# Kernel tuning notes

Hardware: AMD Instinct MI355X
Metric: run time of the kernel (lower is better)

The kernel has to match this reference:

```python
import jax, jax.numpy as jnp
import numpy as np

N_NODES = 100000


def gcn_conv(x, edge_index, W, b):
    # PyG GCNConv: add self-loops, symmetric normalization, then scatter-add.
    n = x.shape[0]
    loops = jnp.arange(n, dtype=edge_index.dtype)
    src = jnp.concatenate([edge_index[0], loops])
    dst = jnp.concatenate([edge_index[1], loops])
    h = x @ W  # [N, F_out] -- transform before propagate (small GEMM)
    ones = jnp.ones(src.shape[0], dtype=x.dtype)
    deg = jax.ops.segment_sum(ones, dst, num_segments=n)  # in-degree incl. self-loop
    dinv = jnp.where(deg > 0, jax.lax.rsqrt(deg), 0.0)
    norm = dinv[src] * dinv[dst]  # [E+N]
    msg = h[src] * norm[:, None]  # gather + scale, [E+N, F_out]
    out = jax.ops.segment_sum(msg, dst, num_segments=n)  # scatter-add
    return out + b


def setup_inputs() -> dict:
    key = jax.random.key(0)
    k1, k2, k3, k4 = jax.random.split(key, 4)
    d = 128
    x = jax.random.normal(k1, (N_NODES, d), dtype=jnp.float32)
    edge_index = jax.random.randint(k2, (2, 1600000), 0, N_NODES, dtype=jnp.int64)
    scale = 1.0 / np.sqrt(d)
    W1 = jax.random.normal(k3, (d, d), dtype=jnp.float32) * scale
    b1 = jnp.zeros((d,), dtype=jnp.float32)
    W2 = jax.random.normal(k4, (d, d), dtype=jnp.float32) * scale
    b2 = jnp.zeros((d,), dtype=jnp.float32)
    return {"x": x, "edge_index": edge_index, "W1": W1, "b1": b1, "W2": W2, "b2": b2}


def reference(x, edge_index, W1, b1, W2, b2):
    # Layer 1: GCNConv -> relu -> dropout(eval: identity)
    h = jax.nn.relu(gcn_conv(x, edge_index, W1, b1))
    # Layer 2
    h = jax.nn.relu(gcn_conv(h, edge_index, W2, b2))
    return h
```

## Files before the change

### kernel.cpp

```cpp
#include <hip/hip_runtime.h>


#define NFEAT 128
#define BSH 7
#define MAXNB 1024
#define BCAP 4096
#define HP 72

typedef __attribute__((ext_vector_type(8))) short s8v;
typedef __attribute__((ext_vector_type(4))) float f4v;
typedef __attribute__((ext_vector_type(2))) float f2v;
typedef __attribute__((ext_vector_type(4))) uint u4v;

__device__ inline ushort f2bf(float f) {
    union { float f; uint u; } x; x.f = f;
    uint u = x.u;
    return (ushort)((u + 0x7fffu + ((u >> 16) & 1u)) >> 16);
}
__device__ inline f2v unpk(uint u) {
    union { uint u; float f; } lo, hi;
    lo.u = u << 16;
    hi.u = u & 0xffff0000u;
    return (f2v){lo.f, hi.f};
}
__device__ inline void upfma2(uint4 v, float g, f2v* a) {
    a[0] += g * unpk(v.x);
    a[1] += g * unpk(v.y);
    a[2] += g * unpk(v.z);
    a[3] += g * unpk(v.w);
}

template <bool ABF16>
__device__ inline void gemm_body(ushort* Bs, int bid, const void* __restrict__ Ap,
                                 const float* __restrict__ W,
                                 ushort* __restrict__ hs, int M) {
    int t = threadIdx.x;
    int w = t >> 6, l = t & 63;
    int q = l >> 4, ln = l & 15;
    int row0 = (bid * 4 + w) * 16;

    int arow = row0 + ln;
    if (arow >= M) arow = M - 1;
    s8v afr[4];
    if (ABF16) {
        const ushort* A = (const ushort*)Ap + (size_t)arow * NFEAT + q * 8;
#pragma unroll
        for (int g = 0; g < 4; g++) afr[g] = *(const s8v*)(A + g * 32);
    } else {
        const float* A = (const float*)Ap + (size_t)arow * NFEAT + q * 8;
#pragma unroll
        for (int g = 0; g < 4; g++) {
            float4 f0 = *(const float4*)(A + g * 32);
            float4 f1 = *(const float4*)(A + g * 32 + 4);
            ushort o[8] = {f2bf(f0.x), f2bf(f0.y), f2bf(f0.z), f2bf(f0.w),
                           f2bf(f1.x), f2bf(f1.y), f2bf(f1.z), f2bf(f1.w)};
            __builtin_memcpy(&afr[g], o, 16);
        }
    }

    f4v acc[8];
#pragma unroll
    for (int nt = 0; nt < 8; nt++) acc[nt] = (f4v){0.f, 0.f, 0.f, 0.f};

#pragma unroll
    for (int h = 0; h < 2; h++) {
        if (h) __syncthreads();
#pragma unroll
        for (int i = 0; i < 8; i++) {
            int idx = t + i * 256;
            int k4 = idx >> 7;
            int n = idx & 127;
            ushort o[4];
#pragma unroll
            for (int j = 0; j < 4; j++) o[j] = f2bf(W[(h * 64 + k4 * 4 + j) * NFEAT + n]);
            uint2 pk;
            __builtin_memcpy(&pk, o, 8);
            *(uint2*)&Bs[n * HP + k4 * 4] = pk;
        }
        __syncthreads();
#pragma unroll
        for (int nt = 0; nt < 8; nt++) {
            const ushort* Bp = Bs + (nt * 16 + ln) * HP + q * 8;
#pragma unroll
            for (int ks = 0; ks < 2; ks++) {
                s8v bfr = *(const s8v*)(Bp + ks * 32);
                acc[nt] = __builtin_amdgcn_mfma_f32_16x16x32_bf16(afr[h * 2 + ks], bfr, acc[nt], 0, 0, 0);
            }
        }
    }

#pragma unroll
    for (int r = 0; r < 4; r++) {
        int row = row0 + q * 4 + r;
        if (row < M) {
            ushort* hp = hs + (size_t)row * NFEAT + ln;
#pragma unroll
            for (int nt = 0; nt < 8; nt++) hp[nt * 16] = f2bf(acc[nt][r]);
        }
    }
}

__global__ __launch_bounds__(256) void k_fused1(const int* __restrict__ src,
                                                const int* __restrict__ dst,
                                                int* __restrict__ gcnt,
                                                uint* __restrict__ ebuf,
                                                int E, int NB, int CH, int chBlk,
                                                const float* __restrict__ x,
                                                const float* __restrict__ W1,
                                                ushort* __restrict__ hs, int M) {
    __shared__ __align__(16) ushort smem[128 * HP];
    int bid = blockIdx.x;
    int sid = bid / 3, r = bid % 3;
    if (r == 0 && sid < chBlk) {
        int* h = (int*)smem;
        int t = threadIdx.x;
        for (int i = t; i < NB; i += 256) h[i] = 0;
        __syncthreads();
        int e0 = sid * CH;
        int e1 = min(e0 + CH, E);
        for (int e = e0 + t; e < e1; e += 256) atomicAdd(&h[dst[e] >> BSH], 1);
        __syncthreads();
        for (int i = t; i < NB; i += 256) {
            int c = h[i];
            h[i] = c ? (i * BCAP + atomicAdd(&gcnt[i], c)) : 0;
        }
        __syncthreads();
        for (int e = e0 + t; e < e1; e += 256) {
            int d = dst[e];
            int b = d >> BSH;
            int p = atomicAdd(&h[b], 1);
            if (p < (b + 1) * BCAP)
                ebuf[p] = ((uint)src[e] << BSH) | (uint)(d & ((1 << BSH) - 1));
        }
    } else {
        int scats_before = min(sid + (r ? 1 : 0), chBlk);
        gemm_body<false>(smem, bid - scats_before, x, W1, hs, M);
    }
}

template <bool ABF16>
__global__ __launch_bounds__(256) void k_gemm3(const void* __restrict__ Ap,
                                               const float* __restrict__ W,
                                               ushort* __restrict__ hs, int M) {
    __shared__ __align__(16) ushort Bs[128 * HP];
    gemm_body<ABF16>(Bs, blockIdx.x, Ap, W, hs, M);
}

__global__ __launch_bounds__(256) void k_fill2(const uint* __restrict__ ebuf,
                                               const int* __restrict__ gcnt,
                                               int* __restrict__ row_ptr,
                                               float* __restrict__ dinv,
                                               int* __restrict__ col,
                                               int N, int E, int NB) {
    __shared__ int cnt[128];
    __shared__ int pre[128];
    __shared__ int sred[256];
    __shared__ int colL[BCAP];
    int b = blockIdx.x;
    int t = threadIdx.x;
    int part = 0;
    for (int j = t; j < b; j += 256) part += gcnt[j];
    sred[t] = part;
    __syncthreads();
    for (int off = 128; off >= 1; off >>= 1) {
        if (t < off) sred[t] += sred[t + off];
        __syncthreads();
    }
    int gb = sred[0];
    int m = min(gcnt[b], BCAP);
    if (t < 128) cnt[t] = 0;
    __syncthreads();
    const uint* eb = ebuf + (size_t)b * BCAP;
    for (int i = t; i < m; i += 256) atomicAdd(&cnt[eb[i] & 127], 1);
    __syncthreads();
    if (t < 128) pre[t] = cnt[t];
    __syncthreads();
    for (int off = 1; off < 128; off <<= 1) {
        int add = (t >= off && t < 128) ? pre[t - off] : 0;
        __syncthreads();
        if (t < 128) pre[t] += add;
        __syncthreads();
    }
    if (t < 128) {
        pre[t] -= cnt[t];
        int node = (b << BSH) + t;
        if (node < N) {
            row_ptr[node] = gb + pre[t];
            dinv[node] = rsqrtf((float)(cnt[t] + 1));
        }
    }
    __syncthreads();
    for (int i = t; i < m; i += 256) {
        uint p = eb[i];
        int pos = atomicAdd(&pre[p & 127], 1);
        colL[pos] = (int)(p >> BSH);
    }
    __syncthreads();
    for (int i = t; i < m; i += 256) col[gb + i] = colL[i];
    if (b == NB - 1 && t == 0) row_ptr[N] = E;
}

template <bool OUT_BF16>
__global__ __launch_bounds__(256) void k_aggregate(const uint4* __restrict__ hs4,
                                                   const int* __restrict__ row_ptr,
                                                   const int* __restrict__ col,
                                                   const float* __restrict__ dinv,
                                                   const float* __restrict__ bias,
                                                   void* __restrict__ outp, int N) {
    int node = blockIdx.x * 16 + (threadIdx.x >> 4);
    if (node >= N) return;
    int sub = threadIdx.x & 15;

    uint4 vself = hs4[(size_t)node * 16 + sub];
    float dself = dinv[node];
    int s = row_ptr[node], e = row_ptr[node + 1];
    int nb = (e - s) >> 2;

    f2v a[4];
#pragma unroll
    for (int j = 0; j < 4; j++) a[j] = (f2v){0.f, 0.f};

    int k = s;
    if (nb > 0) {
        int c0 = col[k], c1 = col[k + 1], c2 = col[k + 2], c3 = col[k + 3];
        uint4 v0 = hs4[(size_t)c0 * 16 + sub];
        uint4 v1 = hs4[(size_t)c1 * 16 + sub];
        uint4 v2 = hs4[(size_t)c2 * 16 + sub];
        uint4 v3 = hs4[(size_t)c3 * 16 + sub];
        float g0 = dinv[c0], g1 = dinv[c1], g2 = dinv[c2], g3 = dinv[c3];
        int d0 = col[k + 4], d1 = col[k + 5], d2 = col[k + 6], d3 = col[k + 7];
        k += 8;
        upfma2(vself, dself, a);
        for (int it = 1; it < nb; ++it, k += 4) {
            uint4 w0 = hs4[(size_t)d0 * 16 + sub];
            uint4 w1 = hs4[(size_t)d1 * 16 + sub];
            uint4 w2 = hs4[(size_t)d2 * 16 + sub];
            uint4 w3 = hs4[(size_t)d3 * 16 + sub];
            float h0 = dinv[d0], h1 = dinv[d1], h2 = dinv[d2], h3 = dinv[d3];
            int t0 = col[k], t1 = col[k + 1], t2 = col[k + 2], t3 = col[k + 3];
            upfma2(v0, g0, a); upfma2(v1, g1, a); upfma2(v2, g2, a); upfma2(v3, g3, a);
            v0 = w0; v1 = w1; v2 = w2; v3 = w3;
            g0 = h0; g1 = h1; g2 = h2; g3 = h3;
            d0 = t0; d1 = t1; d2 = t2; d3 = t3;
        }
        upfma2(v0, g0, a); upfma2(v1, g1, a); upfma2(v2, g2, a); upfma2(v3, g3, a);
        k = s + nb * 4;
    } else {
        upfma2(vself, dself, a);
    }
    for (; k < e; ++k) {
        int c = col[k];
        upfma2(hs4[(size_t)c * 16 + sub], dinv[c], a);
    }

    float di = dinv[node];
    const float4* b4 = (const float4*)bias;
    float4 b0 = b4[sub * 2], b1 = b4[sub * 2 + 1];
    float r[8];
    r[0] = fmaxf(fmaf(di, a[0].x, b0.x), 0.f);
    r[1] = fmaxf(fmaf(di, a[0].y, b0.y), 0.f);
    r[2] = fmaxf(fmaf(di, a[1].x, b0.z), 0.f);
    r[3] = fmaxf(fmaf(di, a[1].y, b0.w), 0.f);
    r[4] = fmaxf(fmaf(di, a[2].x, b1.x), 0.f);
    r[5] = fmaxf(fmaf(di, a[2].y, b1.y), 0.f);
    r[6] = fmaxf(fmaf(di, a[3].x, b1.z), 0.f);
    r[7] = fmaxf(fmaf(di, a[3].y, b1.w), 0.f);
    if (OUT_BF16) {
        ushort o[8];
#pragma unroll
        for (int j = 0; j < 8; j++) o[j] = f2bf(r[j]);
        u4v pk;
        __builtin_memcpy(&pk, o, 16);
        __builtin_nontemporal_store(pk, (u4v*)outp + (size_t)node * 16 + sub);
    } else {
        float* orow = (float*)outp + (size_t)node * NFEAT + sub * 8;
        f4v r0 = {r[0], r[1], r[2], r[3]};
        f4v r1 = {r[4], r[5], r[6], r[7]};
        __builtin_nontemporal_store(r0, (f4v*)orow);
        __builtin_nontemporal_store(r1, (f4v*)(orow + 4));
    }
}

extern "C" void kernel_launch(void* const* d_in, const int* in_sizes, int n_in,
                              void* d_out, int out_size, void* d_ws, size_t ws_size,
                              hipStream_t stream) {
    const float* x = (const float*)d_in[0];
    const int* ei = (const int*)d_in[1];
    const float* W1 = (const float*)d_in[2];
    const float* b1 = (const float*)d_in[3];
    const float* W2 = (const float*)d_in[4];
    const float* b2 = (const float*)d_in[5];
    float* out = (float*)d_out;

    const int N = in_sizes[0] / NFEAT;
    const int E = in_sizes[1] / 2;
    const int* src = ei;
    const int* dst = ei + E;
    const int NB = (N + (1 << BSH) - 1) >> BSH;

    char* w = (char*)d_ws;
    size_t off = 0;
    auto alloc = [&](size_t bytes) -> void* {
        void* p = w + off;
        off = (off + bytes + 511) & ~(size_t)511;
        return p;
    };
    ushort* hs = (ushort*)alloc((size_t)N * NFEAT * 2);
    ushort* y1 = (ushort*)alloc((size_t)N * NFEAT * 2);
    int* row_ptr = (int*)alloc((size_t)(N + 1) * 4);
    float* dinv = (float*)alloc((size_t)N * 4);
    int* col = (int*)alloc((size_t)(E + 64) * 4);
    uint* ebuf = (uint*)alloc((size_t)NB * BCAP * 4);
    int* gcnt = (int*)alloc((size_t)MAXNB * 4);
    (void)ws_size; (void)n_in; (void)out_size;

    const int CH = 2048;
    const int chBlk = (E + CH - 1) / CH;
    const int gemmBlk = (N + 63) / 64;
    const int aggBlk = (N + 15) / 16;

    hipMemsetAsync(gcnt, 0, (size_t)MAXNB * 4, stream);
    k_fused1<<<chBlk + gemmBlk, 256, 0, stream>>>(src, dst, gcnt, ebuf, E, NB, CH, chBlk,
                                                  x, W1, hs, N);
    k_fill2<<<NB, 256, 0, stream>>>(ebuf, gcnt, row_ptr, dinv, col, N, E, NB);

    k_aggregate<true><<<aggBlk, 256, 0, stream>>>((const uint4*)hs, row_ptr, col, dinv, b1, y1, N);
    k_gemm3<true><<<gemmBlk, 256, 0, stream>>>(y1, W2, hs, N);
    k_aggregate<false><<<aggBlk, 256, 0, stream>>>((const uint4*)hs, row_ptr, col, dinv, b2, out, N);
}
```

Before: 306.1 us.

## Fuse layer-1 aggregation with layer-2 GEMM through shared memory

```diff
diff --git a/kernel.cpp b/kernel.cpp
--- a/kernel.cpp
+++ b/kernel.cpp
@@ -6,6 +6,7 @@
 #define MAXNB 1024
 #define BCAP 4096
 #define HP 72
+#define YP 132
 
 typedef __attribute__((ext_vector_type(8))) short s8v;
 typedef __attribute__((ext_vector_type(4))) float f4v;
@@ -30,196 +31,15 @@
     a[3] += g * unpk(v.w);
 }
 
-template <bool ABF16>
-__device__ inline void gemm_body(ushort* Bs, int bid, const void* __restrict__ Ap,
-                                 const float* __restrict__ W,
-                                 ushort* __restrict__ hs, int M) {
-    int t = threadIdx.x;
-    int w = t >> 6, l = t & 63;
-    int q = l >> 4, ln = l & 15;
-    int row0 = (bid * 4 + w) * 16;
-
-    int arow = row0 + ln;
-    if (arow >= M) arow = M - 1;
-    s8v afr[4];
-    if (ABF16) {
-        const ushort* A = (const ushort*)Ap + (size_t)arow * NFEAT + q * 8;
-#pragma unroll
-        for (int g = 0; g < 4; g++) afr[g] = *(const s8v*)(A + g * 32);
-    } else {
-        const float* A = (const float*)Ap + (size_t)arow * NFEAT + q * 8;
-#pragma unroll
-        for (int g = 0; g < 4; g++) {
-            float4 f0 = *(const float4*)(A + g * 32);
-            float4 f1 = *(const float4*)(A + g * 32 + 4);
-            ushort o[8] = {f2bf(f0.x), f2bf(f0.y), f2bf(f0.z), f2bf(f0.w),
-                           f2bf(f1.x), f2bf(f1.y), f2bf(f1.z), f2bf(f1.w)};
-            __builtin_memcpy(&afr[g], o, 16);
-        }
-    }
-
-    f4v acc[8];
-#pragma unroll
-    for (int nt = 0; nt < 8; nt++) acc[nt] = (f4v){0.f, 0.f, 0.f, 0.f};
-
-#pragma unroll
-    for (int h = 0; h < 2; h++) {
-        if (h) __syncthreads();
-#pragma unroll
-        for (int i = 0; i < 8; i++) {
-            int idx = t + i * 256;
-            int k4 = idx >> 7;
-            int n = idx & 127;
-            ushort o[4];
-#pragma unroll
-            for (int j = 0; j < 4; j++) o[j] = f2bf(W[(h * 64 + k4 * 4 + j) * NFEAT + n]);
-            uint2 pk;
-            __builtin_memcpy(&pk, o, 8);
-            *(uint2*)&Bs[n * HP + k4 * 4] = pk;
-        }
-        __syncthreads();
-#pragma unroll
-        for (int nt = 0; nt < 8; nt++) {
-            const ushort* Bp = Bs + (nt * 16 + ln) * HP + q * 8;
-#pragma unroll
-            for (int ks = 0; ks < 2; ks++) {
-                s8v bfr = *(const s8v*)(Bp + ks * 32);
-                acc[nt] = __builtin_amdgcn_mfma_f32_16x16x32_bf16(afr[h * 2 + ks], bfr, acc[nt], 0, 0, 0);
-            }
-        }
-    }
-
-#pragma unroll
-    for (int r = 0; r < 4; r++) {
-        int row = row0 + q * 4 + r;
-        if (row < M) {
-            ushort* hp = hs + (size_t)row * NFEAT + ln;
-#pragma unroll
-            for (int nt = 0; nt < 8; nt++) hp[nt * 16] = f2bf(acc[nt][r]);
-        }
-    }
-}
-
-__global__ __launch_bounds__(256) void k_fused1(const int* __restrict__ src,
-                                                const int* __restrict__ dst,
-                                                int* __restrict__ gcnt,
-                                                uint* __restrict__ ebuf,
-                                                int E, int NB, int CH, int chBlk,
-                                                const float* __restrict__ x,
-                                                const float* __restrict__ W1,
-                                                ushort* __restrict__ hs, int M) {
-    __shared__ __align__(16) ushort smem[128 * HP];
-    int bid = blockIdx.x;
-    int sid = bid / 3, r = bid % 3;
-    if (r == 0 && sid < chBlk) {
-        int* h = (int*)smem;
-        int t = threadIdx.x;
-        for (int i = t; i < NB; i += 256) h[i] = 0;
-        __syncthreads();
-        int e0 = sid * CH;
-        int e1 = min(e0 + CH, E);
-        for (int e = e0 + t; e < e1; e += 256) atomicAdd(&h[dst[e] >> BSH], 1);
-        __syncthreads();
-        for (int i = t; i < NB; i += 256) {
-            int c = h[i];
-            h[i] = c ? (i * BCAP + atomicAdd(&gcnt[i], c)) : 0;
-        }
-        __syncthreads();
-        for (int e = e0 + t; e < e1; e += 256) {
-            int d = dst[e];
-            int b = d >> BSH;
-            int p = atomicAdd(&h[b], 1);
-            if (p < (b + 1) * BCAP)
-                ebuf[p] = ((uint)src[e] << BSH) | (uint)(d & ((1 << BSH) - 1));
-        }
-    } else {
-        int scats_before = min(sid + (r ? 1 : 0), chBlk);
-        gemm_body<false>(smem, bid - scats_before, x, W1, hs, M);
-    }
-}
-
-template <bool ABF16>
-__global__ __launch_bounds__(256) void k_gemm3(const void* __restrict__ Ap,
-                                               const float* __restrict__ W,
-                                               ushort* __restrict__ hs, int M) {
-    __shared__ __align__(16) ushort Bs[128 * HP];
-    gemm_body<ABF16>(Bs, blockIdx.x, Ap, W, hs, M);
-}
-
-__global__ __launch_bounds__(256) void k_fill2(const uint* __restrict__ ebuf,
-                                               const int* __restrict__ gcnt,
-                                               int* __restrict__ row_ptr,
-                                               float* __restrict__ dinv,
-                                               int* __restrict__ col,
-                                               int N, int E, int NB) {
-    __shared__ int cnt[128];
-    __shared__ int pre[128];
-    __shared__ int sred[256];
-    __shared__ int colL[BCAP];
-    int b = blockIdx.x;
-    int t = threadIdx.x;
-    int part = 0;
-    for (int j = t; j < b; j += 256) part += gcnt[j];
-    sred[t] = part;
-    __syncthreads();
-    for (int off = 128; off >= 1; off >>= 1) {
-        if (t < off) sred[t] += sred[t + off];
-        __syncthreads();
-    }
-    int gb = sred[0];
-    int m = min(gcnt[b], BCAP);
-    if (t < 128) cnt[t] = 0;
-    __syncthreads();
-    const uint* eb = ebuf + (size_t)b * BCAP;
-    for (int i = t; i < m; i += 256) atomicAdd(&cnt[eb[i] & 127], 1);
-    __syncthreads();
-    if (t < 128) pre[t] = cnt[t];
-    __syncthreads();
-    for (int off = 1; off < 128; off <<= 1) {
-        int add = (t >= off && t < 128) ? pre[t - off] : 0;
-        __syncthreads();
-        if (t < 128) pre[t] += add;
-        __syncthreads();
-    }
-    if (t < 128) {
-        pre[t] -= cnt[t];
-        int node = (b << BSH) + t;
-        if (node < N) {
-            row_ptr[node] = gb + pre[t];
-            dinv[node] = rsqrtf((float)(cnt[t] + 1));
-        }
-    }
-    __syncthreads();
-    for (int i = t; i < m; i += 256) {
-        uint p = eb[i];
-        int pos = atomicAdd(&pre[p & 127], 1);
-        colL[pos] = (int)(p >> BSH);
-    }
-    __syncthreads();
-    for (int i = t; i < m; i += 256) col[gb + i] = colL[i];
-    if (b == NB - 1 && t == 0) row_ptr[N] = E;
-}
-
-template <bool OUT_BF16>
-__global__ __launch_bounds__(256) void k_aggregate(const uint4* __restrict__ hs4,
-                                                   const int* __restrict__ row_ptr,
-                                                   const int* __restrict__ col,
-                                                   const float* __restrict__ dinv,
-                                                   const float* __restrict__ bias,
-                                                   void* __restrict__ outp, int N) {
-    int node = blockIdx.x * 16 + (threadIdx.x >> 4);
-    if (node >= N) return;
-    int sub = threadIdx.x & 15;
-
+__device__ inline void node_gather(const uint4* __restrict__ hs4,
+                                   const int* __restrict__ row_ptr,
+                                   const int* __restrict__ col,
+                                   const float* __restrict__ dinv,
+                                   int node, int sub, f2v* a) {
     uint4 vself = hs4[(size_t)node * 16 + sub];
     float dself = dinv[node];
     int s = row_ptr[node], e = row_ptr[node + 1];
     int nb = (e - s) >> 2;
-
-    f2v a[4];
-#pragma unroll
-    for (int j = 0; j < 4; j++) a[j] = (f2v){0.f, 0.f};
-
     int k = s;
     if (nb > 0) {
         int c0 = col[k], c1 = col[k + 1], c2 = col[k + 2], c3 = col[k + 3];
@@ -252,6 +72,264 @@
         int c = col[k];
         upfma2(hs4[(size_t)c * 16 + sub], dinv[c], a);
     }
+}
+
+__device__ inline void stage_w_half(ushort* Bs, const float* __restrict__ W, int h, int t) {
+#pragma unroll
+    for (int i = 0; i < 8; i++) {
+        int idx = t + i * 256;
+        int k4 = idx >> 7;
+        int n = idx & 127;
+        ushort o[4];
+#pragma unroll
+        for (int j = 0; j < 4; j++) o[j] = f2bf(W[(h * 64 + k4 * 4 + j) * NFEAT + n]);
+        uint2 pk;
+        __builtin_memcpy(&pk, o, 8);
+        *(uint2*)&Bs[n * HP + k4 * 4] = pk;
+    }
+}
+
+template <bool ABF16>
+__device__ inline void gemm_body(ushort* Bs, int bid, const void* __restrict__ Ap,
+                                 const float* __restrict__ W,
+                                 ushort* __restrict__ hs, int M) {
+    int t = threadIdx.x;
+    int w = t >> 6, l = t & 63;
+    int q = l >> 4, ln = l & 15;
+    int row0 = (bid * 4 + w) * 16;
+
+    int arow = row0 + ln;
+    if (arow >= M) arow = M - 1;
+    s8v afr[4];
+    if (ABF16) {
+        const ushort* A = (const ushort*)Ap + (size_t)arow * NFEAT + q * 8;
+#pragma unroll
+        for (int g = 0; g < 4; g++) afr[g] = *(const s8v*)(A + g * 32);
+    } else {
+        const float* A = (const float*)Ap + (size_t)arow * NFEAT + q * 8;
+#pragma unroll
+        for (int g = 0; g < 4; g++) {
+            float4 f0 = *(const float4*)(A + g * 32);
+            float4 f1 = *(const float4*)(A + g * 32 + 4);
+            ushort o[8] = {f2bf(f0.x), f2bf(f0.y), f2bf(f0.z), f2bf(f0.w),
+                           f2bf(f1.x), f2bf(f1.y), f2bf(f1.z), f2bf(f1.w)};
+            __builtin_memcpy(&afr[g], o, 16);
+        }
+    }
+
+    f4v acc[8];
+#pragma unroll
+    for (int nt = 0; nt < 8; nt++) acc[nt] = (f4v){0.f, 0.f, 0.f, 0.f};
+
+#pragma unroll
+    for (int h = 0; h < 2; h++) {
+        if (h) __syncthreads();
+        stage_w_half(Bs, W, h, t);
+        __syncthreads();
+#pragma unroll
+        for (int nt = 0; nt < 8; nt++) {
+            const ushort* Bp = Bs + (nt * 16 + ln) * HP + q * 8;
+#pragma unroll
+            for (int ks = 0; ks < 2; ks++) {
+                s8v bfr = *(const s8v*)(Bp + ks * 32);
+                acc[nt] = __builtin_amdgcn_mfma_f32_16x16x32_bf16(afr[h * 2 + ks], bfr, acc[nt], 0, 0, 0);
+            }
+        }
+    }
+
+#pragma unroll
+    for (int r = 0; r < 4; r++) {
+        int row = row0 + q * 4 + r;
+        if (row < M) {
+            ushort* hp = hs + (size_t)row * NFEAT + ln;
+#pragma unroll
+            for (int nt = 0; nt < 8; nt++) hp[nt * 16] = f2bf(acc[nt][r]);
+        }
+    }
+}
+
+__global__ __launch_bounds__(256) void k_fused1(const int* __restrict__ src,
+                                                const int* __restrict__ dst,
+                                                int* __restrict__ gcnt,
+                                                uint* __restrict__ ebuf,
+                                                int E, int NB, int CH, int chBlk,
+                                                const float* __restrict__ x,
+                                                const float* __restrict__ W1,
+                                                ushort* __restrict__ hs, int M) {
+    __shared__ __align__(16) ushort smem[128 * HP];
+    int bid = blockIdx.x;
+    int sid = bid / 3, r = bid % 3;
+    if (r == 0 && sid < chBlk) {
+        int* h = (int*)smem;
+        int t = threadIdx.x;
+        for (int i = t; i < NB; i += 256) h[i] = 0;
+        __syncthreads();
+        int e0 = sid * CH;
+        int e1 = min(e0 + CH, E);
+        for (int e = e0 + t; e < e1; e += 256) atomicAdd(&h[dst[e] >> BSH], 1);
+        __syncthreads();
+        for (int i = t; i < NB; i += 256) {
+            int c = h[i];
+            h[i] = c ? (i * BCAP + atomicAdd(&gcnt[i], c)) : 0;
+        }
+        __syncthreads();
+        for (int e = e0 + t; e < e1; e += 256) {
+            int d = dst[e];
+            int b = d >> BSH;
+            int p = atomicAdd(&h[b], 1);
+            if (p < (b + 1) * BCAP)
+                ebuf[p] = ((uint)src[e] << BSH) | (uint)(d & ((1 << BSH) - 1));
+        }
+    } else {
+        int scats_before = min(sid + (r ? 1 : 0), chBlk);
+        gemm_body<false>(smem, bid - scats_before, x, W1, hs, M);
+    }
+}
+
+__global__ __launch_bounds__(256) void k_fill2(const uint* __restrict__ ebuf,
+                                               const int* __restrict__ gcnt,
+                                               int* __restrict__ row_ptr,
+                                               float* __restrict__ dinv,
+                                               int* __restrict__ col,
+                                               int N, int E, int NB) {
+    __shared__ int cnt[128];
+    __shared__ int pre[128];
+    __shared__ int sred[256];
+    __shared__ int colL[BCAP];
+    int b = blockIdx.x;
+    int t = threadIdx.x;
+    int part = 0;
+    for (int j = t; j < b; j += 256) part += gcnt[j];
+    sred[t] = part;
+    __syncthreads();
+    for (int off = 128; off >= 1; off >>= 1) {
+        if (t < off) sred[t] += sred[t + off];
+        __syncthreads();
+    }
+    int gb = sred[0];
+    int m = min(gcnt[b], BCAP);
+    if (t < 128) cnt[t] = 0;
+    __syncthreads();
+    const uint* eb = ebuf + (size_t)b * BCAP;
+    for (int i = t; i < m; i += 256) atomicAdd(&cnt[eb[i] & 127], 1);
+    __syncthreads();
+    if (t < 128) pre[t] = cnt[t];
+    __syncthreads();
+    for (int off = 1; off < 128; off <<= 1) {
+        int add = (t >= off && t < 128) ? pre[t - off] : 0;
+        __syncthreads();
+        if (t < 128) pre[t] += add;
+        __syncthreads();
+    }
+    if (t < 128) {
+        pre[t] -= cnt[t];
+        int node = (b << BSH) + t;
+        if (node < N) {
+            row_ptr[node] = gb + pre[t];
+            dinv[node] = rsqrtf((float)(cnt[t] + 1));
+        }
+    }
+    __syncthreads();
+    for (int i = t; i < m; i += 256) {
+        uint p = eb[i];
+        int pos = atomicAdd(&pre[p & 127], 1);
+        colL[pos] = (int)(p >> BSH);
+    }
+    __syncthreads();
+    for (int i = t; i < m; i += 256) col[gb + i] = colL[i];
+    if (b == NB - 1 && t == 0) row_ptr[N] = E;
+}
+
+__global__ __launch_bounds__(256) void k_aggG(const uint4* __restrict__ hs4,
+                                              const int* __restrict__ row_ptr,
+                                              const int* __restrict__ col,
+                                              const float* __restrict__ dinv,
+                                              const float* __restrict__ bias,
+                                              const float* __restrict__ W2,
+                                              ushort* __restrict__ hs2, int N) {
+    __shared__ __align__(16) ushort yT[64 * YP];
+    __shared__ __align__(16) ushort Bs[128 * HP];
+    int t = threadIdx.x;
+    int grp = t >> 4, sub = t & 15;
+    int base = blockIdx.x * 64;
+
+    const float4* b4 = (const float4*)bias;
+    float4 bb0 = b4[sub * 2], bb1 = b4[sub * 2 + 1];
+
+    for (int i = 0; i < 4; i++) {
+        int myn = grp + i * 16;
+        int node = base + myn;
+        uint4 pk = make_uint4(0, 0, 0, 0);
+        if (node < N) {
+            f2v a[4];
+#pragma unroll
+            for (int j = 0; j < 4; j++) a[j] = (f2v){0.f, 0.f};
+            node_gather(hs4, row_ptr, col, dinv, node, sub, a);
+            float di = dinv[node];
+            ushort o[8];
+            o[0] = f2bf(fmaxf(fmaf(di, a[0].x, bb0.x), 0.f));
+            o[1] = f2bf(fmaxf(fmaf(di, a[0].y, bb0.y), 0.f));
+            o[2] = f2bf(fmaxf(fmaf(di, a[1].x, bb0.z), 0.f));
+            o[3] = f2bf(fmaxf(fmaf(di, a[1].y, bb0.w), 0.f));
+            o[4] = f2bf(fmaxf(fmaf(di, a[2].x, bb1.x), 0.f));
+            o[5] = f2bf(fmaxf(fmaf(di, a[2].y, bb1.y), 0.f));
+            o[6] = f2bf(fmaxf(fmaf(di, a[3].x, bb1.z), 0.f));
+            o[7] = f2bf(fmaxf(fmaf(di, a[3].y, bb1.w), 0.f));
+            __builtin_memcpy(&pk, o, 16);
+        }
+        *(uint4*)&yT[myn * YP + sub * 8] = pk;
+    }
+    __syncthreads();
+
+    int w = t >> 6, l = t & 63;
+    int q = l >> 4, ln = l & 15;
+    f4v acc[8];
+#pragma unroll
+    for (int nt = 0; nt < 8; nt++) acc[nt] = (f4v){0.f, 0.f, 0.f, 0.f};
+#pragma unroll
+    for (int h = 0; h < 2; h++) {
+        if (h) __syncthreads();
+        stage_w_half(Bs, W2, h, t);
+        __syncthreads();
+        s8v a2[2];
+        a2[0] = *(const s8v*)&yT[(w * 16 + ln) * YP + (h * 2 + 0) * 32 + q * 8];
+        a2[1] = *(const s8v*)&yT[(w * 16 + ln) * YP + (h * 2 + 1) * 32 + q * 8];
+#pragma unroll
+        for (int nt = 0; nt < 8; nt++) {
+            const ushort* Bp = Bs + (nt * 16 + ln) * HP + q * 8;
+#pragma unroll
+            for (int ks = 0; ks < 2; ks++) {
+                s8v bfr = *(const s8v*)(Bp + ks * 32);
+                acc[nt] = __builtin_amdgcn_mfma_f32_16x16x32_bf16(a2[ks], bfr, acc[nt], 0, 0, 0);
+            }
+        }
+    }
+#pragma unroll
+    for (int rr = 0; rr < 4; rr++) {
+        int node = base + w * 16 + q * 4 + rr;
+        if (node < N) {
+            ushort* hp = hs2 + (size_t)node * NFEAT + ln;
+#pragma unroll
+            for (int nt = 0; nt < 8; nt++) hp[nt * 16] = f2bf(acc[nt][rr]);
+        }
+    }
+}
+
+template <bool OUT_BF16>
+__global__ __launch_bounds__(256) void k_aggregate(const uint4* __restrict__ hs4,
+                                                   const int* __restrict__ row_ptr,
+                                                   const int* __restrict__ col,
+                                                   const float* __restrict__ dinv,
+                                                   const float* __restrict__ bias,
+                                                   void* __restrict__ outp, int N) {
+    int node = blockIdx.x * 16 + (threadIdx.x >> 4);
+    if (node >= N) return;
+    int sub = threadIdx.x & 15;
+
+    f2v a[4];
+#pragma unroll
+    for (int j = 0; j < 4; j++) a[j] = (f2v){0.f, 0.f};
+    node_gather(hs4, row_ptr, col, dinv, node, sub, a);
 
     float di = dinv[node];
     const float4* b4 = (const float4*)bias;
@@ -306,7 +384,7 @@
         return p;
     };
     ushort* hs = (ushort*)alloc((size_t)N * NFEAT * 2);
-    ushort* y1 = (ushort*)alloc((size_t)N * NFEAT * 2);
+    ushort* hs2 = (ushort*)alloc((size_t)N * NFEAT * 2);
     int* row_ptr = (int*)alloc((size_t)(N + 1) * 4);
     float* dinv = (float*)alloc((size_t)N * 4);
     int* col = (int*)alloc((size_t)(E + 64) * 4);
@@ -324,7 +402,6 @@
                                                   x, W1, hs, N);
     k_fill2<<<NB, 256, 0, stream>>>(ebuf, gcnt, row_ptr, dinv, col, N, E, NB);
 
-    k_aggregate<true><<<aggBlk, 256, 0, stream>>>((const uint4*)hs, row_ptr, col, dinv, b1, y1, N);
-    k_gemm3<true><<<gemmBlk, 256, 0, stream>>>(y1, W2, hs, N);
-    k_aggregate<false><<<aggBlk, 256, 0, stream>>>((const uint4*)hs, row_ptr, col, dinv, b2, out, N);
-}
+    k_aggG<<<gemmBlk, 256, 0, stream>>>((const uint4*)hs, row_ptr, col, dinv, b1, W2, hs2, N);
+    k_aggregate<false><<<aggBlk, 256, 0, stream>>>((const uint4*)hs2, row_ptr, col, dinv, b2, out, N);
+}
```

After: 307.1 us. About the same (+0.3%).
